# Kernel tuning notes

Hardware: AMD Instinct MI355X
Metric: run time of the kernel (lower is better)

Reference implementation:

```python
import jax, jax.numpy as jnp
import numpy as np

NUM_HEAD_CHANNELS = 64
GROUPS = 32
EPS = 1e-5


def setup_inputs() -> dict:
    key = jax.random.key(0)
    ks = jax.random.split(key, 3)
    B, C, H, W = 16, 512, 64, 64
    x = jax.random.normal(ks[0], (B, C, H, W), jnp.float32)
    gn_gamma = jnp.ones((C,), jnp.float32)
    gn_beta = jnp.zeros((C,), jnp.float32)
    # 1x1 conv weights (out_ch, in_ch); fan-in scaling keeps softmax logits sane
    w_qkv = jax.random.normal(ks[1], (3 * C, C), jnp.float32) / np.float32(np.sqrt(C))
    b_qkv = jnp.zeros((3 * C,), jnp.float32)
    w_proj = jax.random.normal(ks[2], (C, C), jnp.float32) / np.float32(np.sqrt(C))
    b_proj = jnp.zeros((C,), jnp.float32)
    return dict(x=x, gn_gamma=gn_gamma, gn_beta=gn_beta, w_qkv=w_qkv,
                b_qkv=b_qkv, w_proj=w_proj, b_proj=b_proj)


def _group_norm(x, gamma, beta):
    B, C, H, W = x.shape
    xg = x.reshape(B, GROUPS, C // GROUPS, H, W)
    mu = xg.mean(axis=(2, 3, 4), keepdims=True)
    var = xg.var(axis=(2, 3, 4), keepdims=True)
    xn = ((xg - mu) * jax.lax.rsqrt(var + EPS)).reshape(B, C, H, W)
    return xn * gamma[None, :, None, None] + beta[None, :, None, None]


def reference(x, gn_gamma, gn_beta, w_qkv, b_qkv, w_proj, b_proj):
    B, C, H, W = x.shape
    L = H * W
    heads = C // NUM_HEAD_CHANNELS
    Lh = L // heads  # module splits spatial length across heads

    xn = _group_norm(x, gn_gamma, gn_beta).reshape(B, C, L)
    # 1x1 conv QKV: (3C, C) x (B, C, L) -> (B, 3C, L)
    qkv = jnp.einsum('oc,bcl->bol', w_qkv, xn) + b_qkv[None, :, None]
    qkv = qkv.reshape(B, 3 * C, heads, Lh)
    q, k, v = jnp.split(qkv, 3, axis=1)  # each (B, C, heads, Lh)

    scale = np.float32(1.0 / np.sqrt(C // heads))
    w_att = jnp.einsum('bchq,bchk->bhqk', q * scale, k)  # (B, heads, Lh, Lh)
    w_att = jax.nn.softmax(w_att.astype(jnp.float32), axis=-1).astype(q.dtype)
    a = jnp.einsum('bhqk,bchk->bchq', w_att, v)  # (B, C, heads, Lh)
    a = a.reshape(B, C, L)  # contiguous reinterpretation, as torch .view

    out = jnp.einsum('oc,bcl->bol', w_proj, a) + b_proj[None, :, None]
    return x + out.reshape(B, C, H, W)
```

## Files before the change

kernel.cpp:

```cpp
#include <hip/hip_runtime.h>

typedef unsigned short u16;
typedef __attribute__((ext_vector_type(8))) short bf16x8;
typedef __attribute__((ext_vector_type(4))) short bf16x4;
typedef __attribute__((ext_vector_type(4))) float f32x4;

__device__ __forceinline__ float bf2f(u16 u){ union { unsigned int i; float f; } v; v.i = ((unsigned int)u) << 16; return v.f; }
__device__ __forceinline__ u16 f2bf(float f){ union { float f; unsigned int i; } v; v.f = f; unsigned int r = v.i + 0x7fffu + ((v.i >> 16) & 1u); return (u16)(r >> 16); }

#define MFMA(a,b,c) __builtin_amdgcn_mfma_f32_16x16x32_bf16((a),(b),(c),0,0,0)

__device__ __forceinline__ void gl_lds16(const u16* g, u16* l){
  __builtin_amdgcn_global_load_lds((const __attribute__((address_space(1))) unsigned int*)g,
                                   (__attribute__((address_space(3))) unsigned int*)l, 16, 0, 0);
}

__global__ __launch_bounds__(256) void k_gn_stats(const float* __restrict__ x, float* __restrict__ stats){
  const int bg = blockIdx.x;
  const float4* p = (const float4*)(x + (size_t)bg * 65536);
  const int tid = threadIdx.x;
  float s = 0.f, sq = 0.f;
  for (int i = 0; i < 64; ++i){
    float4 v = p[tid + i*256];
    s += v.x + v.y + v.z + v.w;
    sq += v.x*v.x + v.y*v.y + v.z*v.z + v.w*v.w;
  }
#pragma unroll
  for (int d = 32; d > 0; d >>= 1){ s += __shfl_down(s, d, 64); sq += __shfl_down(sq, d, 64); }
  __shared__ float ls[4], lq[4];
  if ((tid & 63) == 0){ ls[tid>>6] = s; lq[tid>>6] = sq; }
  __syncthreads();
  if (tid == 0){
    float S = ls[0]+ls[1]+ls[2]+ls[3];
    float Q = lq[0]+lq[1]+lq[2]+lq[3];
    float mean = S * (1.f/65536.f);
    float var  = Q * (1.f/65536.f) - mean*mean;
    stats[bg*2]   = mean;
    stats[bg*2+1] = rsqrtf(var + 1e-5f);
  }
}

__global__ __launch_bounds__(256) void k_conv_w(const float* __restrict__ wq, const float* __restrict__ wp,
                                                u16* __restrict__ wout){
  const int base = (blockIdx.x*256 + threadIdx.x) * 4;
  float4 v;
  if (base < 786432) v = *(const float4*)(wq + base);
  else               v = *(const float4*)(wp + (base - 786432));
  bf16x4 o;
  o[0] = (short)f2bf(v.x); o[1] = (short)f2bf(v.y); o[2] = (short)f2bf(v.z); o[3] = (short)f2bf(v.w);
  *(bf16x4*)(wout + base) = o;
}

__global__ __launch_bounds__(256) void k_gn_t(const float* __restrict__ x, const float* __restrict__ stats,
                                              const float* __restrict__ gamma, const float* __restrict__ beta,
                                              u16* __restrict__ xnt){
  __shared__ u16 tile[64*72];
  const int l0 = blockIdx.x*64, c0 = blockIdx.y*64, b = blockIdx.z;
  const int tid = threadIdx.x;
#pragma unroll
  for (int i = 0; i < 2; ++i){
    int v = tid + i*256; int cc = v >> 3, seg = v & 7;
    int c = c0 + cc;
    float mu = stats[(b*32 + (c>>4))*2], rs = stats[(b*32 + (c>>4))*2 + 1];
    float ga = gamma[c] * rs;
    float be = beta[c] - mu * ga;
    const float* px = x + ((size_t)(b*512 + c))*4096 + l0 + seg*8;
    float4 a0 = *(const float4*)px;
    float4 a1 = *(const float4*)(px + 4);
    bf16x8 ov;
    ov[0]=(short)f2bf(a0.x*ga+be); ov[1]=(short)f2bf(a0.y*ga+be);
    ov[2]=(short)f2bf(a0.z*ga+be); ov[3]=(short)f2bf(a0.w*ga+be);
    ov[4]=(short)f2bf(a1.x*ga+be); ov[5]=(short)f2bf(a1.y*ga+be);
    ov[6]=(short)f2bf(a1.z*ga+be); ov[7]=(short)f2bf(a1.w*ga+be);
    *(bf16x8*)&tile[cc*72 + seg*8] = ov;
  }
  __syncthreads();
#pragma unroll
  for (int i = 0; i < 2; ++i){
    int v = tid + i*256; int ll = v >> 3, seg = v & 7;
    bf16x8 ov;
#pragma unroll
    for (int j = 0; j < 8; ++j) ov[j] = (short)tile[(seg*8 + j)*72 + ll];
    *(bf16x8*)(xnt + ((size_t)(b*4096 + l0 + ll))*512 + c0 + seg*8) = ov;
  }
}

__global__ __launch_bounds__(256,3) void k_qkv(const u16* __restrict__ xnt, const u16* __restrict__ wq,
                                               const float* __restrict__ bq,
                                               u16* __restrict__ Qt, u16* __restrict__ Kt, u16* __restrict__ Vh){
  __shared__ u16 smem[24576];
  const int l0 = blockIdx.x*128, o0 = blockIdx.y*128, b = blockIdx.z;
  const int tid = threadIdx.x, wv = tid>>6, lane = tid&63, g = lane>>4, r = lane&15;
  const int wm = wv>>1, wn = wv&1;
  const u16* Ab = xnt + ((size_t)(b*4096 + l0))*512;
  const u16* Wb = wq  + (size_t)o0*512;
  const u16* gsrc[4];
  int ldoff[4];
#pragma unroll
  for (int j = 0; j < 4; ++j){
    const int s = j*256 + tid;
    const int row = s >> 2, pc = s & 3;
    const int lc = pc ^ ((row >> 1) & 3);
    gsrc[j] = ((row < 128) ? (Ab + (size_t)row*512) : (Wb + (size_t)(row - 128)*512)) + lc*8;
    ldoff[j] = (j*256 + wv*64)*8;
  }
  f32x4 acc[4][4];
#pragma unroll
  for (int mt = 0; mt < 4; ++mt)
#pragma unroll
    for (int nt = 0; nt < 4; ++nt) acc[mt][nt] = (f32x4){0.f,0.f,0.f,0.f};

#define STG3(bufo, c0) do { \
    u16* _bb = smem + (bufo); \
    _Pragma("unroll") \
    for (int _j = 0; _j < 4; ++_j) gl_lds16(gsrc[_j] + (c0), _bb + ldoff[_j]); \
  } while(0)

#define CMP3(bufo) do { \
    const u16* _cb = smem + (bufo); \
    const int _sw = (g ^ ((r >> 1) & 3)) * 8; \
    bf16x8 a_[4], w_[4]; \
    _Pragma("unroll") \
    for (int _mt = 0; _mt < 4; ++_mt) a_[_mt] = *(const bf16x8*)&_cb[(wm*64 + _mt*16 + r)*32 + _sw]; \
    _Pragma("unroll") \
    for (int _nt = 0; _nt < 4; ++_nt) w_[_nt] = *(const bf16x8*)&_cb[4096 + (wn*64 + _nt*16 + r)*32 + _sw]; \
    __builtin_amdgcn_s_setprio(1); \
    _Pragma("unroll") \
    for (int _mt = 0; _mt < 4; ++_mt) \
      _Pragma("unroll") \
      for (int _nt = 0; _nt < 4; ++_nt) acc[_mt][_nt] = MFMA(a_[_mt], w_[_nt], acc[_mt][_nt]); \
    __builtin_amdgcn_s_setprio(0); \
  } while(0)

  STG3(0,     0);
  STG3(8192, 32);
  int cur = 0;
  for (int cs = 0; cs < 14; ++cs){
    asm volatile("s_waitcnt vmcnt(4)" ::: "memory");
    __builtin_amdgcn_s_barrier();
    __builtin_amdgcn_sched_barrier(0);
    int bn = cur + 2; if (bn >= 3) bn -= 3;
    STG3(bn*8192, (cs + 2)*32);
    CMP3(cur*8192);
    if (++cur == 3) cur = 0;
  }
  asm volatile("s_waitcnt vmcnt(4)" ::: "memory");
  __builtin_amdgcn_s_barrier();
  __builtin_amdgcn_sched_barrier(0);
  CMP3(cur*8192);
  if (++cur == 3) cur = 0;
  asm volatile("s_waitcnt vmcnt(0)" ::: "memory");
  __builtin_amdgcn_s_barrier();
  __builtin_amdgcn_sched_barrier(0);
  CMP3(cur*8192);
#undef STG3
#undef CMP3

  __syncthreads();
  const int t   = blockIdx.y >> 2;
  const int cp0 = (blockIdx.y & 3)*128;
  const int h   = blockIdx.x >> 2;
  const int lh0 = (blockIdx.x & 3)*128;
#pragma unroll
  for (int nt = 0; nt < 4; ++nt){
    const int ol = wn*64 + nt*16 + r;
    const float bi = bq[o0 + ol];
#pragma unroll
    for (int mt = 0; mt < 4; ++mt){
      const int ll = wm*64 + mt*16 + g*4;
      if (t == 2){
        bf16x4 pk;
#pragma unroll
        for (int rr = 0; rr < 4; ++rr) pk[rr] = (short)f2bf(acc[mt][nt][rr] + bi);
        *(bf16x4*)&smem[ol*136 + ll] = pk;
      } else {
#pragma unroll
        for (int rr = 0; rr < 4; ++rr) smem[(ll + rr)*136 + ol] = f2bf(acc[mt][nt][rr] + bi);
      }
    }
  }
  __syncthreads();
  const size_t bh = (size_t)(b*8 + h);
  u16* dst = (t == 0) ? Qt : Kt;
#pragma unroll
  for (int i = 0; i < 8; ++i){
    int v = tid + i*256; int row = v >> 4, seg = v & 15;
    bf16x8 d = *(const bf16x8*)&smem[row*136 + seg*8];
    if (t == 2){
      *(bf16x8*)(Vh + (bh*512 + cp0 + row)*512 + lh0 + seg*8) = d;
    } else {
      *(bf16x8*)(dst + (bh*512 + lh0 + row)*512 + cp0 + seg*8) = d;
    }
  }
}

__global__ __launch_bounds__(512,2) void k_attn(const u16* __restrict__ Qt, const u16* __restrict__ Kt,
                                                const u16* __restrict__ Vh, u16* __restrict__ At){
  extern __shared__ __align__(16) u16 smem[];
  float* sMax = (float*)(smem + 65536);
  float* sSum = sMax + 512;
  const int wgid = blockIdx.x;
  const int orig = (wgid & 7)*64 + (wgid >> 3);
  const int b = orig >> 5, h = (orig >> 2) & 7, q0 = (orig & 3) * 128;
  const int bh = b*8 + h;
  const int tid = threadIdx.x, wv = tid>>6, lane = tid&63, g = lane>>4, r = lane&15;
  const int wq = wv>>2, wk = wv&3;
  const size_t base = (size_t)bh * 262144;
  const u16* Qb = Qt + base + (size_t)q0*512;
  const u16* Kb = Kt + base;
  const u16* Vb = Vh + base;

  const u16* gsrc[5];
  int ldoff[5];
  {
    const int l4 = lane >> 2, pc = lane & 3;
#pragma unroll
    for (int j = 0; j < 5; ++j){
      const int i = wv*5 + j;
      const int row = ((i < 8) ? (i*16) : ((i-8)*16)) + l4;
      const u16* bp = (i < 8) ? (Qb + (size_t)row*512) : (Kb + (size_t)row*512);
      gsrc[j] = bp + ((pc ^ ((row >> 1) & 3)) * 8);
      ldoff[j] = i * 512;
    }
  }

  f32x4 s[4][8];
#pragma unroll
  for (int mt = 0; mt < 4; ++mt)
#pragma unroll
    for (int nt = 0; nt < 8; ++nt) s[mt][nt] = (f32x4){0.f,0.f,0.f,0.f};

  const int qswz = (g ^ ((r >> 1) & 3)) * 8;

#define STAGE_QK(bufbase, c0) do { \
    u16* _bb = (bufbase); \
    _Pragma("unroll") \
    for (int _j = 0; _j < 5; ++_j) gl_lds16(gsrc[_j] + (c0), _bb + ldoff[_j]); \
  } while(0)

#define QK_COMPUTE(bbp) do { \
    const u16* _cb = (bbp); \
    bf16x8 a_[4], kb_[8]; \
    _Pragma("unroll") \
    for (int _mt = 0; _mt < 4; ++_mt) a_[_mt] = *(const bf16x8*)&_cb[(wq*64 + _mt*16 + r)*32 + qswz]; \
    _Pragma("unroll") \
    for (int _nt = 0; _nt < 8; ++_nt) kb_[_nt] = *(const bf16x8*)&_cb[4096 + (wk*128 + _nt*16 + r)*32 + qswz]; \
    __builtin_amdgcn_s_setprio(1); \
    _Pragma("unroll") \
    for (int _mt = 0; _mt < 4; ++_mt) \
      _Pragma("unroll") \
      for (int _nt = 0; _nt < 8; ++_nt) s[_mt][_nt] = MFMA(a_[_mt], kb_[_nt], s[_mt][_nt]); \
    __builtin_amdgcn_s_setprio(0); \
  } while(0)

  STAGE_QK(smem,         0);
  STAGE_QK(smem + 20480, 32);
  int bcur = 0;
  for (int cs = 0; cs < 15; ++cs){
    asm volatile("s_waitcnt vmcnt(5)" ::: "memory");
    __builtin_amdgcn_s_barrier();
    __builtin_amdgcn_sched_barrier(0);
    if (cs < 14){
      int bn = bcur + 2; if (bn >= 3) bn -= 3;
      STAGE_QK(smem + bn*20480, (cs+2)*32);
    }
    QK_COMPUTE(smem + bcur*20480);
    if (++bcur == 3) bcur = 0;
  }
  asm volatile("s_waitcnt vmcnt(0)" ::: "memory");
  __builtin_amdgcn_s_barrier();
  __builtin_amdgcn_sched_barrier(0);
  QK_COMPUTE(smem + bcur*20480);

#pragma unroll
  for (int mt = 0; mt < 4; ++mt)
#pragma unroll
    for (int nt = 0; nt < 8; ++nt)
#pragma unroll
      for (int rr = 0; rr < 4; ++rr) s[mt][nt][rr] *= 0.125f;

  float mx[4][4];
#pragma unroll
  for (int mt = 0; mt < 4; ++mt)
#pragma unroll
    for (int rr = 0; rr < 4; ++rr){
      float m = s[mt][0][rr];
#pragma unroll
      for (int nt = 1; nt < 8; ++nt) m = fmaxf(m, s[mt][nt][rr]);
      m = fmaxf(m, __shfl_xor(m, 1, 64)); m = fmaxf(m, __shfl_xor(m, 2, 64));
      m = fmaxf(m, __shfl_xor(m, 4, 64)); m = fmaxf(m, __shfl_xor(m, 8, 64));
      mx[mt][rr] = m;
    }
  if (r == 0){
#pragma unroll
    for (int mt = 0; mt < 4; ++mt)
#pragma unroll
      for (int rr = 0; rr < 4; ++rr) sMax[(wq*64 + mt*16 + g*4 + rr)*4 + wk] = mx[mt][rr];
  }
  __syncthreads();
#pragma unroll
  for (int mt = 0; mt < 4; ++mt)
#pragma unroll
    for (int rr = 0; rr < 4; ++rr){
      float4 v = *(const float4*)&sMax[(wq*64 + mt*16 + g*4 + rr)*4];
      mx[mt][rr] = fmaxf(fmaxf(v.x, v.y), fmaxf(v.z, v.w));
    }
  float inv[4][4];
#pragma unroll
  for (int mt = 0; mt < 4; ++mt)
#pragma unroll
    for (int rr = 0; rr < 4; ++rr){
      float t = 0.f;
#pragma unroll
      for (int nt = 0; nt < 8; ++nt){
        float e = __expf(s[mt][nt][rr] - mx[mt][rr]);
        s[mt][nt][rr] = e; t += e;
      }
      t += __shfl_xor(t, 1, 64); t += __shfl_xor(t, 2, 64);
      t += __shfl_xor(t, 4, 64); t += __shfl_xor(t, 8, 64);
      inv[mt][rr] = t;
    }
  if (r == 0){
#pragma unroll
    for (int mt = 0; mt < 4; ++mt)
#pragma unroll
      for (int rr = 0; rr < 4; ++rr) sSum[(wq*64 + mt*16 + g*4 + rr)*4 + wk] = inv[mt][rr];
  }
  __syncthreads();
#pragma unroll
  for (int mt = 0; mt < 4; ++mt)
#pragma unroll
    for (int rr = 0; rr < 4; ++rr){
      float4 v = *(const float4*)&sSum[(wq*64 + mt*16 + g*4 + rr)*4];
      inv[mt][rr] = 1.f / (v.x + v.y + v.z + v.w);
    }
  {
    const int kx7 = r & 7, kbase = wk*16 + (r>>3);
#pragma unroll
    for (int mt = 0; mt < 4; ++mt)
#pragma unroll
      for (int rr = 0; rr < 4; ++rr){
        const int q = wq*64 + mt*16 + g*4 + rr;
        const int ro = q*512, qx = q & 7;
        const float iv = inv[mt][rr];
#pragma unroll
        for (int nt = 0; nt < 8; ++nt){
          const int ch = kbase + nt*2;
          smem[ro + ((ch ^ qx) * 8) + kx7] = f2bf(s[mt][nt][rr] * iv);
        }
      }
  }
  const u16* Vw = Vb + (size_t)(wv*64 + r)*512 + g*8;
  bf16x8 vf[2][4];
#pragma unroll
  for (int mt = 0; mt < 4; ++mt) vf[0][mt] = *(const bf16x8*)(Vw + mt*8192);
  __syncthreads();

  f32x4 o[4][8];
#pragma unroll
  for (int mt = 0; mt < 4; ++mt)
#pragma unroll
    for (int nt = 0; nt < 8; ++nt) o[mt][nt] = (f32x4){0.f,0.f,0.f,0.f};
#pragma unroll
  for (int kk = 0; kk < 16; ++kk){
    if (kk < 15){
#pragma unroll
      for (int mt = 0; mt < 4; ++mt) vf[(kk+1)&1][mt] = *(const bf16x8*)(Vw + mt*8192 + (kk+1)*32);
    }
    bf16x8 pp[8];
#pragma unroll
    for (int nt = 0; nt < 8; ++nt){
      const int q = nt*16 + r;
      pp[nt] = *(const bf16x8*)&smem[q*512 + (((kk*4 + g) ^ (r & 7)) * 8)];
    }
    __builtin_amdgcn_s_setprio(1);
#pragma unroll
    for (int mt = 0; mt < 4; ++mt)
#pragma unroll
      for (int nt = 0; nt < 8; ++nt) o[mt][nt] = MFMA(vf[kk&1][mt], pp[nt], o[mt][nt]);
    __builtin_amdgcn_s_setprio(0);
  }
  __syncthreads();

#pragma unroll
  for (int mt = 0; mt < 4; ++mt){
    const int c = wv*64 + mt*16 + g*4;
    const int ch = c >> 3, cl = c & 7;
#pragma unroll
    for (int nt = 0; nt < 8; ++nt){
      const int q = nt*16 + r;
      bf16x4 pk;
#pragma unroll
      for (int rr = 0; rr < 4; ++rr) pk[rr] = (short)f2bf(o[mt][nt][rr]);
      *(bf16x4*)&smem[q*512 + ((ch ^ (r & 7)) * 8) + cl] = pk;
    }
  }
  __syncthreads();
  u16* Ad = At + ((size_t)(bh*512 + q0))*512;
#pragma unroll
  for (int i = 0; i < 16; ++i){
    const int idx = tid + i*512, q = idx >> 6, ch = idx & 63;
    bf16x8 d = *(const bf16x8*)&smem[q*512 + ((ch ^ (q & 7)) * 8)];
    *(bf16x8*)(Ad + (size_t)q*512 + ch*8) = d;
  }
#undef STAGE_QK
#undef QK_COMPUTE
}

__global__ __launch_bounds__(256,3) void k_proj(const u16* __restrict__ At, const u16* __restrict__ wp,
                                                const float* __restrict__ bpr, const float* __restrict__ x,
                                                float* __restrict__ out){
  __shared__ u16 smem[24576];
  const int l0 = blockIdx.x*128, o0 = blockIdx.y*128, b = blockIdx.z;
  const int tid = threadIdx.x, wv = tid>>6, lane = tid&63, g = lane>>4, r = lane&15;
  const int wm = wv>>1, wn = wv&1;
  const u16* Ab = At + ((size_t)(b*4096 + l0))*512;
  const u16* Wb = wp + (size_t)o0*512;
  const u16* gsrc[4];
  int ldoff[4];
#pragma unroll
  for (int j = 0; j < 4; ++j){
    const int s = j*256 + tid;
    const int row = s >> 2, pc = s & 3;
    const int lc = pc ^ ((row >> 1) & 3);
    gsrc[j] = ((row < 128) ? (Ab + (size_t)row*512) : (Wb + (size_t)(row - 128)*512)) + lc*8;
    ldoff[j] = (j*256 + wv*64)*8;
  }
  f32x4 acc[4][4];
#pragma unroll
  for (int mt = 0; mt < 4; ++mt)
#pragma unroll
    for (int nt = 0; nt < 4; ++nt) acc[mt][nt] = (f32x4){0.f,0.f,0.f,0.f};

#define STG5(bufo, c0) do { \
    u16* _bb = smem + (bufo); \
    _Pragma("unroll") \
    for (int _j = 0; _j < 4; ++_j) gl_lds16(gsrc[_j] + (c0), _bb + ldoff[_j]); \
  } while(0)

#define CMP5(bufo) do { \
    const u16* _cb = smem + (bufo); \
    const int _sw = (g ^ ((r >> 1) & 3)) * 8; \
    bf16x8 a_[4], w_[4]; \
    _Pragma("unroll") \
    for (int _mt = 0; _mt < 4; ++_mt) a_[_mt] = *(const bf16x8*)&_cb[(wm*64 + _mt*16 + r)*32 + _sw]; \
    _Pragma("unroll") \
    for (int _nt = 0; _nt < 4; ++_nt) w_[_nt] = *(const bf16x8*)&_cb[4096 + (wn*64 + _nt*16 + r)*32 + _sw]; \
    __builtin_amdgcn_s_setprio(1); \
    _Pragma("unroll") \
    for (int _mt = 0; _mt < 4; ++_mt) \
      _Pragma("unroll") \
      for (int _nt = 0; _nt < 4; ++_nt) acc[_mt][_nt] = MFMA(a_[_mt], w_[_nt], acc[_mt][_nt]); \
    __builtin_amdgcn_s_setprio(0); \
  } while(0)

  STG5(0,     0);
  STG5(8192, 32);
  int cur = 0;
  for (int cs = 0; cs < 14; ++cs){
    asm volatile("s_waitcnt vmcnt(4)" ::: "memory");
    __builtin_amdgcn_s_barrier();
    __builtin_amdgcn_sched_barrier(0);
    int bn = cur + 2; if (bn >= 3) bn -= 3;
    STG5(bn*8192, (cs + 2)*32);
    CMP5(cur*8192);
    if (++cur == 3) cur = 0;
  }
  asm volatile("s_waitcnt vmcnt(4)" ::: "memory");
  __builtin_amdgcn_s_barrier();
  __builtin_amdgcn_sched_barrier(0);
  CMP5(cur*8192);
  if (++cur == 3) cur = 0;
  asm volatile("s_waitcnt vmcnt(0)" ::: "memory");
  __builtin_amdgcn_s_barrier();
  __builtin_amdgcn_sched_barrier(0);
  CMP5(cur*8192);
#undef STG5
#undef CMP5

  __syncthreads();
#pragma unroll
  for (int nt = 0; nt < 4; ++nt){
    const int ol = wn*64 + nt*16 + r;
    const float bi = bpr[o0 + ol];
#pragma unroll
    for (int mt = 0; mt < 4; ++mt){
      const int ll = wm*64 + mt*16 + g*4;
      bf16x4 pk;
#pragma unroll
      for (int rr = 0; rr < 4; ++rr) pk[rr] = (short)f2bf(acc[mt][nt][rr] + bi);
      *(bf16x4*)&smem[ol*136 + ll] = pk;
    }
  }
  __syncthreads();
#pragma unroll
  for (int i = 0; i < 16; ++i){
    int v = tid + i*256; int row = v >> 5, seg = v & 31;
    bf16x4 d = *(const bf16x4*)&smem[row*136 + seg*4];
    const size_t gi = ((size_t)(b*512 + o0 + row))*4096 + l0 + seg*4;
    float4 xv = *(const float4*)(x + gi);
    float4 ov;
    ov.x = bf2f((u16)d[0]) + xv.x;
    ov.y = bf2f((u16)d[1]) + xv.y;
    ov.z = bf2f((u16)d[2]) + xv.z;
    ov.w = bf2f((u16)d[3]) + xv.w;
    *(float4*)(out + gi) = ov;
  }
}

extern "C" void kernel_launch(void* const* d_in, const int* in_sizes, int n_in,
                              void* d_out, int out_size, void* d_ws, size_t ws_size,
                              hipStream_t stream) {
  (void)in_sizes; (void)n_in; (void)out_size; (void)ws_size;
  const float* x     = (const float*)d_in[0];
  const float* gamma = (const float*)d_in[1];
  const float* beta  = (const float*)d_in[2];
  const float* wqkv  = (const float*)d_in[3];
  const float* bqkv  = (const float*)d_in[4];
  const float* wproj = (const float*)d_in[5];
  const float* bproj = (const float*)d_in[6];
  float* out = (float*)d_out;
  char* ws = (char*)d_ws;

  float* stats = (float*)ws;
  u16* W16  = (u16*)(ws + 8192);
  u16* Wq16 = W16;
  u16* Wp16 = W16 + 786432;
  u16* Qt = (u16*)(ws + 8192 + 2097152);
  u16* Kt = Qt + (size_t)33554432;
  u16* Vh = Kt + (size_t)33554432;
  u16* At = Qt;
  u16* Xnt = (u16*)d_out;

  static bool attn_attr = false;
  if (!attn_attr){
    hipFuncSetAttribute((const void*)k_attn, hipFuncAttributeMaxDynamicSharedMemorySize, 135168);
    attn_attr = true;
  }

  k_gn_stats<<<512, 256, 0, stream>>>(x, stats);
  k_conv_w<<<1024, 256, 0, stream>>>(wqkv, wproj, W16);
  k_gn_t<<<dim3(64,8,16), 256, 0, stream>>>(x, stats, gamma, beta, Xnt);
  k_qkv<<<dim3(32,12,16), 256, 0, stream>>>(Xnt, Wq16, bqkv, Qt, Kt, Vh);
  k_attn<<<512, 512, 135168, stream>>>(Qt, Kt, Vh, At);
  k_proj<<<dim3(32,4,16), 256, 0, stream>>>(At, Wp16, bproj, x, out);
}
```

Before: 565.0 us.

## Enlarge QKV and projection GEMM tiles to 256x256 with 512-thread blocks

Doubles the output tile of the QKV and output-projection GEMMs from 128x128 to 256x256, using 8 waves per block that each compute a 128x64 sub-tile. This cuts global and LDS traffic per MFMA and roughly quarters the block count. The staging buffers move to 96KB of dynamic LDS, and the epilogue is split into two half-tile passes through LDS so it fits. The cost is fewer blocks (1536 and 512), lower occupancy, more accumulator registers, and extra barriers in the epilogue.

```diff
diff --git a/kernel.cpp b/kernel.cpp
--- a/kernel.cpp
+++ b/kernel.cpp
@@ -85,28 +85,28 @@
   }
 }
 
-__global__ __launch_bounds__(256,3) void k_qkv(const u16* __restrict__ xnt, const u16* __restrict__ wq,
+__global__ __launch_bounds__(512,2) void k_qkv(const u16* __restrict__ xnt, const u16* __restrict__ wq,
                                                const float* __restrict__ bq,
                                                u16* __restrict__ Qt, u16* __restrict__ Kt, u16* __restrict__ Vh){
-  __shared__ u16 smem[24576];
-  const int l0 = blockIdx.x*128, o0 = blockIdx.y*128, b = blockIdx.z;
+  extern __shared__ __align__(16) u16 smem[];
+  const int l0 = blockIdx.x*256, o0 = blockIdx.y*256, b = blockIdx.z;
   const int tid = threadIdx.x, wv = tid>>6, lane = tid&63, g = lane>>4, r = lane&15;
-  const int wm = wv>>1, wn = wv&1;
+  const int wm = wv>>2, wn = wv&3;
   const u16* Ab = xnt + ((size_t)(b*4096 + l0))*512;
   const u16* Wb = wq  + (size_t)o0*512;
   const u16* gsrc[4];
   int ldoff[4];
 #pragma unroll
   for (int j = 0; j < 4; ++j){
-    const int s = j*256 + tid;
+    const int s = j*512 + tid;
     const int row = s >> 2, pc = s & 3;
     const int lc = pc ^ ((row >> 1) & 3);
-    gsrc[j] = ((row < 128) ? (Ab + (size_t)row*512) : (Wb + (size_t)(row - 128)*512)) + lc*8;
-    ldoff[j] = (j*256 + wv*64)*8;
-  }
-  f32x4 acc[4][4];
-#pragma unroll
-  for (int mt = 0; mt < 4; ++mt)
+    gsrc[j] = ((row < 256) ? (Ab + (size_t)row*512) : (Wb + (size_t)(row - 256)*512)) + lc*8;
+    ldoff[j] = (j*512 + wv*64)*8;
+  }
+  f32x4 acc[8][4];
+#pragma unroll
+  for (int mt = 0; mt < 8; ++mt)
 #pragma unroll
     for (int nt = 0; nt < 4; ++nt) acc[mt][nt] = (f32x4){0.f,0.f,0.f,0.f};
 
@@ -119,77 +119,101 @@
 #define CMP3(bufo) do { \
     const u16* _cb = smem + (bufo); \
     const int _sw = (g ^ ((r >> 1) & 3)) * 8; \
-    bf16x8 a_[4], w_[4]; \
-    _Pragma("unroll") \
-    for (int _mt = 0; _mt < 4; ++_mt) a_[_mt] = *(const bf16x8*)&_cb[(wm*64 + _mt*16 + r)*32 + _sw]; \
-    _Pragma("unroll") \
-    for (int _nt = 0; _nt < 4; ++_nt) w_[_nt] = *(const bf16x8*)&_cb[4096 + (wn*64 + _nt*16 + r)*32 + _sw]; \
+    bf16x8 a_[8], w_[4]; \
+    _Pragma("unroll") \
+    for (int _mt = 0; _mt < 8; ++_mt) a_[_mt] = *(const bf16x8*)&_cb[(wm*128 + _mt*16 + r)*32 + _sw]; \
+    _Pragma("unroll") \
+    for (int _nt = 0; _nt < 4; ++_nt) w_[_nt] = *(const bf16x8*)&_cb[(256 + wn*64 + _nt*16 + r)*32 + _sw]; \
     __builtin_amdgcn_s_setprio(1); \
     _Pragma("unroll") \
-    for (int _mt = 0; _mt < 4; ++_mt) \
+    for (int _mt = 0; _mt < 8; ++_mt) \
       _Pragma("unroll") \
       for (int _nt = 0; _nt < 4; ++_nt) acc[_mt][_nt] = MFMA(a_[_mt], w_[_nt], acc[_mt][_nt]); \
     __builtin_amdgcn_s_setprio(0); \
   } while(0)
 
-  STG3(0,     0);
-  STG3(8192, 32);
+  STG3(0,      0);
+  STG3(16384, 32);
   int cur = 0;
   for (int cs = 0; cs < 14; ++cs){
     asm volatile("s_waitcnt vmcnt(4)" ::: "memory");
     __builtin_amdgcn_s_barrier();
     __builtin_amdgcn_sched_barrier(0);
     int bn = cur + 2; if (bn >= 3) bn -= 3;
-    STG3(bn*8192, (cs + 2)*32);
-    CMP3(cur*8192);
+    STG3(bn*16384, (cs + 2)*32);
+    CMP3(cur*16384);
     if (++cur == 3) cur = 0;
   }
   asm volatile("s_waitcnt vmcnt(4)" ::: "memory");
   __builtin_amdgcn_s_barrier();
   __builtin_amdgcn_sched_barrier(0);
-  CMP3(cur*8192);
+  CMP3(cur*16384);
   if (++cur == 3) cur = 0;
   asm volatile("s_waitcnt vmcnt(0)" ::: "memory");
   __builtin_amdgcn_s_barrier();
   __builtin_amdgcn_sched_barrier(0);
-  CMP3(cur*8192);
+  CMP3(cur*16384);
 #undef STG3
 #undef CMP3
 
   __syncthreads();
-  const int t   = blockIdx.y >> 2;
-  const int cp0 = (blockIdx.y & 3)*128;
-  const int h   = blockIdx.x >> 2;
-  const int lh0 = (blockIdx.x & 3)*128;
-#pragma unroll
-  for (int nt = 0; nt < 4; ++nt){
-    const int ol = wn*64 + nt*16 + r;
-    const float bi = bq[o0 + ol];
-#pragma unroll
-    for (int mt = 0; mt < 4; ++mt){
-      const int ll = wm*64 + mt*16 + g*4;
-      if (t == 2){
-        bf16x4 pk;
-#pragma unroll
-        for (int rr = 0; rr < 4; ++rr) pk[rr] = (short)f2bf(acc[mt][nt][rr] + bi);
-        *(bf16x4*)&smem[ol*136 + ll] = pk;
-      } else {
-#pragma unroll
-        for (int rr = 0; rr < 4; ++rr) smem[(ll + rr)*136 + ol] = f2bf(acc[mt][nt][rr] + bi);
-      }
-    }
-  }
-  __syncthreads();
+  const int t   = blockIdx.y >> 1;
+  const int cp0 = (blockIdx.y & 1)*256;
+  const int h   = blockIdx.x >> 1;
+  const int lh0 = (blockIdx.x & 1)*256;
   const size_t bh = (size_t)(b*8 + h);
-  u16* dst = (t == 0) ? Qt : Kt;
-#pragma unroll
-  for (int i = 0; i < 8; ++i){
-    int v = tid + i*256; int row = v >> 4, seg = v & 15;
-    bf16x8 d = *(const bf16x8*)&smem[row*136 + seg*8];
-    if (t == 2){
-      *(bf16x8*)(Vh + (bh*512 + cp0 + row)*512 + lh0 + seg*8) = d;
-    } else {
-      *(bf16x8*)(dst + (bh*512 + lh0 + row)*512 + cp0 + seg*8) = d;
+  if (t < 2){
+    u16* dst = (t == 0) ? Qt : Kt;
+#pragma unroll
+    for (int p = 0; p < 2; ++p){
+      if (wm == p){
+#pragma unroll
+        for (int nt = 0; nt < 4; ++nt){
+          const int ol = wn*64 + nt*16 + r;
+          const float bi = bq[o0 + ol];
+#pragma unroll
+          for (int mt = 0; mt < 8; ++mt){
+            const int ll = mt*16 + g*4;
+#pragma unroll
+            for (int rr = 0; rr < 4; ++rr) smem[(ll + rr)*264 + ol] = f2bf(acc[mt][nt][rr] + bi);
+          }
+        }
+      }
+      __syncthreads();
+#pragma unroll
+      for (int i = 0; i < 8; ++i){
+        int v = i*512 + tid; int row = v >> 5, seg = v & 31;
+        bf16x8 d = *(const bf16x8*)&smem[row*264 + seg*8];
+        *(bf16x8*)(dst + (bh*512 + lh0 + p*128 + row)*512 + cp0 + seg*8) = d;
+      }
+      __syncthreads();
+    }
+  } else {
+#pragma unroll
+    for (int p = 0; p < 2; ++p){
+      if ((wn >> 1) == p){
+#pragma unroll
+        for (int nt = 0; nt < 4; ++nt){
+          const int ol = (wn & 1)*64 + nt*16 + r;
+          const float bi = bq[o0 + p*128 + ol];
+#pragma unroll
+          for (int mt = 0; mt < 8; ++mt){
+            const int ll = wm*128 + mt*16 + g*4;
+            bf16x4 pk;
+#pragma unroll
+            for (int rr = 0; rr < 4; ++rr) pk[rr] = (short)f2bf(acc[mt][nt][rr] + bi);
+            *(bf16x4*)&smem[ol*264 + ll] = pk;
+          }
+        }
+      }
+      __syncthreads();
+#pragma unroll
+      for (int i = 0; i < 8; ++i){
+        int v = i*512 + tid; int row = v >> 5, seg = v & 31;
+        bf16x8 d = *(const bf16x8*)&smem[row*264 + seg*8];
+        *(bf16x8*)(Vh + (bh*512 + cp0 + p*128 + row)*512 + lh0 + seg*8) = d;
+      }
+      __syncthreads();
     }
   }
 }
@@ -407,28 +431,28 @@
 #undef QK_COMPUTE
 }
 
-__global__ __launch_bounds__(256,3) void k_proj(const u16* __restrict__ At, const u16* __restrict__ wp,
+__global__ __launch_bounds__(512,2) void k_proj(const u16* __restrict__ At, const u16* __restrict__ wp,
                                                 const float* __restrict__ bpr, const float* __restrict__ x,
                                                 float* __restrict__ out){
-  __shared__ u16 smem[24576];
-  const int l0 = blockIdx.x*128, o0 = blockIdx.y*128, b = blockIdx.z;
+  extern __shared__ __align__(16) u16 smem[];
+  const int l0 = blockIdx.x*256, o0 = blockIdx.y*256, b = blockIdx.z;
   const int tid = threadIdx.x, wv = tid>>6, lane = tid&63, g = lane>>4, r = lane&15;
-  const int wm = wv>>1, wn = wv&1;
+  const int wm = wv>>2, wn = wv&3;
   const u16* Ab = At + ((size_t)(b*4096 + l0))*512;
   const u16* Wb = wp + (size_t)o0*512;
   const u16* gsrc[4];
   int ldoff[4];
 #pragma unroll
   for (int j = 0; j < 4; ++j){
-    const int s = j*256 + tid;
+    const int s = j*512 + tid;
     const int row = s >> 2, pc = s & 3;
     const int lc = pc ^ ((row >> 1) & 3);
-    gsrc[j] = ((row < 128) ? (Ab + (size_t)row*512) : (Wb + (size_t)(row - 128)*512)) + lc*8;
-    ldoff[j] = (j*256 + wv*64)*8;
-  }
-  f32x4 acc[4][4];
-#pragma unroll
-  for (int mt = 0; mt < 4; ++mt)
+    gsrc[j] = ((row < 256) ? (Ab + (size_t)row*512) : (Wb + (size_t)(row - 256)*512)) + lc*8;
+    ldoff[j] = (j*512 + wv*64)*8;
+  }
+  f32x4 acc[8][4];
+#pragma unroll
+  for (int mt = 0; mt < 8; ++mt)
 #pragma unroll
     for (int nt = 0; nt < 4; ++nt) acc[mt][nt] = (f32x4){0.f,0.f,0.f,0.f};
 
@@ -441,70 +465,76 @@
 #define CMP5(bufo) do { \
     const u16* _cb = smem + (bufo); \
     const int _sw = (g ^ ((r >> 1) & 3)) * 8; \
-    bf16x8 a_[4], w_[4]; \
-    _Pragma("unroll") \
-    for (int _mt = 0; _mt < 4; ++_mt) a_[_mt] = *(const bf16x8*)&_cb[(wm*64 + _mt*16 + r)*32 + _sw]; \
-    _Pragma("unroll") \
-    for (int _nt = 0; _nt < 4; ++_nt) w_[_nt] = *(const bf16x8*)&_cb[4096 + (wn*64 + _nt*16 + r)*32 + _sw]; \
+    bf16x8 a_[8], w_[4]; \
+    _Pragma("unroll") \
+    for (int _mt = 0; _mt < 8; ++_mt) a_[_mt] = *(const bf16x8*)&_cb[(wm*128 + _mt*16 + r)*32 + _sw]; \
+    _Pragma("unroll") \
+    for (int _nt = 0; _nt < 4; ++_nt) w_[_nt] = *(const bf16x8*)&_cb[(256 + wn*64 + _nt*16 + r)*32 + _sw]; \
     __builtin_amdgcn_s_setprio(1); \
     _Pragma("unroll") \
-    for (int _mt = 0; _mt < 4; ++_mt) \
+    for (int _mt = 0; _mt < 8; ++_mt) \
       _Pragma("unroll") \
       for (int _nt = 0; _nt < 4; ++_nt) acc[_mt][_nt] = MFMA(a_[_mt], w_[_nt], acc[_mt][_nt]); \
     __builtin_amdgcn_s_setprio(0); \
   } while(0)
 
-  STG5(0,     0);
-  STG5(8192, 32);
+  STG5(0,      0);
+  STG5(16384, 32);
   int cur = 0;
   for (int cs = 0; cs < 14; ++cs){
     asm volatile("s_waitcnt vmcnt(4)" ::: "memory");
     __builtin_amdgcn_s_barrier();
     __builtin_amdgcn_sched_barrier(0);
     int bn = cur + 2; if (bn >= 3) bn -= 3;
-    STG5(bn*8192, (cs + 2)*32);
-    CMP5(cur*8192);
+    STG5(bn*16384, (cs + 2)*32);
+    CMP5(cur*16384);
     if (++cur == 3) cur = 0;
   }
   asm volatile("s_waitcnt vmcnt(4)" ::: "memory");
   __builtin_amdgcn_s_barrier();
   __builtin_amdgcn_sched_barrier(0);
-  CMP5(cur*8192);
+  CMP5(cur*16384);
   if (++cur == 3) cur = 0;
   asm volatile("s_waitcnt vmcnt(0)" ::: "memory");
   __builtin_amdgcn_s_barrier();
   __builtin_amdgcn_sched_barrier(0);
-  CMP5(cur*8192);
+  CMP5(cur*16384);
 #undef STG5
 #undef CMP5
 
   __syncthreads();
 #pragma unroll
-  for (int nt = 0; nt < 4; ++nt){
-    const int ol = wn*64 + nt*16 + r;
-    const float bi = bpr[o0 + ol];
-#pragma unroll
-    for (int mt = 0; mt < 4; ++mt){
-      const int ll = wm*64 + mt*16 + g*4;
-      bf16x4 pk;
-#pragma unroll
-      for (int rr = 0; rr < 4; ++rr) pk[rr] = (short)f2bf(acc[mt][nt][rr] + bi);
-      *(bf16x4*)&smem[ol*136 + ll] = pk;
-    }
-  }
-  __syncthreads();
-#pragma unroll
-  for (int i = 0; i < 16; ++i){
-    int v = tid + i*256; int row = v >> 5, seg = v & 31;
-    bf16x4 d = *(const bf16x4*)&smem[row*136 + seg*4];
-    const size_t gi = ((size_t)(b*512 + o0 + row))*4096 + l0 + seg*4;
-    float4 xv = *(const float4*)(x + gi);
-    float4 ov;
-    ov.x = bf2f((u16)d[0]) + xv.x;
-    ov.y = bf2f((u16)d[1]) + xv.y;
-    ov.z = bf2f((u16)d[2]) + xv.z;
-    ov.w = bf2f((u16)d[3]) + xv.w;
-    *(float4*)(out + gi) = ov;
+  for (int p = 0; p < 2; ++p){
+    if ((wn >> 1) == p){
+#pragma unroll
+      for (int nt = 0; nt < 4; ++nt){
+        const int ol = (wn & 1)*64 + nt*16 + r;
+        const float bi = bpr[o0 + p*128 + ol];
+#pragma unroll
+        for (int mt = 0; mt < 8; ++mt){
+          const int ll = wm*128 + mt*16 + g*4;
+          bf16x4 pk;
+#pragma unroll
+          for (int rr = 0; rr < 4; ++rr) pk[rr] = (short)f2bf(acc[mt][nt][rr] + bi);
+          *(bf16x4*)&smem[ol*264 + ll] = pk;
+        }
+      }
+    }
+    __syncthreads();
+#pragma unroll
+    for (int i = 0; i < 16; ++i){
+      int v = i*512 + tid; int row = v >> 6, seg = v & 63;
+      bf16x4 d = *(const bf16x4*)&smem[row*264 + seg*4];
+      const size_t gi = ((size_t)(b*512 + o0 + p*128 + row))*4096 + l0 + seg*4;
+      float4 xv = *(const float4*)(x + gi);
+      float4 ov;
+      ov.x = bf2f((u16)d[0]) + xv.x;
+      ov.y = bf2f((u16)d[1]) + xv.y;
+      ov.z = bf2f((u16)d[2]) + xv.z;
+      ov.w = bf2f((u16)d[3]) + xv.w;
+      *(float4*)(out + gi) = ov;
+    }
+    __syncthreads();
   }
 }
 
@@ -535,13 +565,15 @@
   static bool attn_attr = false;
   if (!attn_attr){
     hipFuncSetAttribute((const void*)k_attn, hipFuncAttributeMaxDynamicSharedMemorySize, 135168);
+    hipFuncSetAttribute((const void*)k_qkv,  hipFuncAttributeMaxDynamicSharedMemorySize, 98304);
+    hipFuncSetAttribute((const void*)k_proj, hipFuncAttributeMaxDynamicSharedMemorySize, 98304);
     attn_attr = true;
   }
 
   k_gn_stats<<<512, 256, 0, stream>>>(x, stats);
   k_conv_w<<<1024, 256, 0, stream>>>(wqkv, wproj, W16);
   k_gn_t<<<dim3(64,8,16), 256, 0, stream>>>(x, stats, gamma, beta, Xnt);
-  k_qkv<<<dim3(32,12,16), 256, 0, stream>>>(Xnt, Wq16, bqkv, Qt, Kt, Vh);
+  k_qkv<<<dim3(16,6,16), 512, 98304, stream>>>(Xnt, Wq16, bqkv, Qt, Kt, Vh);
   k_attn<<<512, 512, 135168, stream>>>(Qt, Kt, Vh, At);
-  k_proj<<<dim3(32,4,16), 256, 0, stream>>>(At, Wp16, bproj, x, out);
-}
+  k_proj<<<dim3(16,2,16), 512, 98304, stream>>>(At, Wp16, bproj, x, out);
+}
```

New measurement: 590.3 us. 1.04x slower.
